# Kernel tuning notes

Hardware: AMD Instinct MI355X
Metric: run time of the kernel (lower is better)

The kernel has to match this reference:

```python
import jax, jax.numpy as jnp
import numpy as np

D = 1024      # hidden_size
FF = 4096     # ff_inner_dim = 4 * D
E = 8         # num_experts
K = 2         # moe_top_k
B, L = 4, 1024


def setup_inputs() -> dict:
    key = jax.random.key(0)
    ks = jax.random.split(key, 12)
    s = 0.02  # weight init scale
    return {
        "x": jax.random.normal(ks[0], (B, L, D), jnp.float32),
        "W_gate": jax.random.normal(ks[1], (D, E), jnp.float32) * s,
        "W1": jax.random.normal(ks[2], (E, D, FF), jnp.float32) * s,
        "b1": jnp.zeros((E, FF), jnp.float32),
        "W2": jax.random.normal(ks[3], (E, FF, D), jnp.float32) * s,
        "b2": jnp.zeros((E, D), jnp.float32),
        "Ws1": jax.random.normal(ks[4], (D, FF), jnp.float32) * s,
        "bs1": jnp.zeros((FF,), jnp.float32),
        "Ws2": jax.random.normal(ks[5], (FF, D), jnp.float32) * s,
        "bs2": jnp.zeros((D,), jnp.float32),
    }


def _gelu(h):
    # torch F.gelu default = exact (erf) gelu
    return jax.nn.gelu(h, approximate=False)


def reference(x, W_gate, W1, b1, W2, b2, Ws1, bs1, Ws2, bs2):
    Bx, Lx, Dx = x.shape
    xf = x.reshape(-1, Dx)                       # [T, D]
    logits = xf @ W_gate                         # [T, E]
    probs = jax.nn.softmax(logits, axis=-1)
    top_v, top_i = jax.lax.top_k(probs, K)       # [T, K]
    top_v = top_v / jnp.sum(top_v, axis=-1, keepdims=True)
    # dense combine weights: [T, E], zero for unselected experts
    combine = jnp.sum(jax.nn.one_hot(top_i, E, dtype=xf.dtype) * top_v[..., None], axis=1)

    out = jnp.zeros_like(xf)
    for e in range(E):  # fixed small expert loop, unrolled under jit
        h = _gelu(xf @ W1[e] + b1[e])            # [T, FF]
        out = out + combine[:, e:e + 1] * (h @ W2[e] + b2[e])

    shared = _gelu(xf @ Ws1 + bs1) @ Ws2 + bs2   # [T, D]
    return (out + shared).reshape(Bx, Lx, Dx)
```

## Files before the change

### kernel.cpp

```cpp
#include <hip/hip_runtime.h>
#include <hip/hip_bf16.h>

typedef unsigned short ushort_t;
typedef __attribute__((ext_vector_type(4))) float f32x4;
typedef __attribute__((ext_vector_type(8))) short bf16x8;
typedef __attribute__((ext_vector_type(8))) unsigned short us8;

#define T_TOK 4096
#define D_DIM 1024
#define FF_DIM 4096
#define NE 8
#define ESTRIDE 4194304L

__device__ __forceinline__ unsigned short f2bf(float f) {
  __hip_bfloat16 h = __float2bfloat16(f);
  return __builtin_bit_cast(unsigned short, h);
}
__device__ __forceinline__ float bf2f(ushort_t u) {
  unsigned int x = ((unsigned int)u) << 16;
  return __builtin_bit_cast(float, x);
}
__device__ __forceinline__ float gelu_f(float v) {
  return 0.5f * v * (1.0f + erff(v * 0.70710678118654752440f));
}

__global__ __launch_bounds__(256) void pre_kernel(
    const float* __restrict__ x, const float* __restrict__ Wg,
    const float* __restrict__ W1, const float* __restrict__ Ws1,
    int* __restrict__ cnt, int* __restrict__ tok,
    float* __restrict__ wof, int* __restrict__ rankof,
    ushort_t* __restrict__ Xbf, ushort_t* __restrict__ W1T) {
  __shared__ ushort_t tile[128][136];
  const int bid = blockIdx.x, tid = threadIdx.x;

  if (bid < 1024) {
    const int t = bid * 4 + (tid >> 6);
    const int lane = tid & 63;
    const float* xr = x + (long)t * D_DIM;
    ushort_t* xb = Xbf + (long)t * D_DIM;
    float acc[NE];
#pragma unroll
    for (int e = 0; e < NE; e++) acc[e] = 0.f;
#pragma unroll
    for (int i = 0; i < 16; i++) {
      int d = i * 64 + lane;
      float xv = xr[d];
      xb[d] = f2bf(xv);
      const float* wr = Wg + d * NE;
#pragma unroll
      for (int e = 0; e < NE; e++) acc[e] += xv * wr[e];
    }
#pragma unroll
    for (int off = 32; off > 0; off >>= 1) {
#pragma unroll
      for (int e = 0; e < NE; e++) acc[e] += __shfl_xor(acc[e], off, 64);
    }
    if (lane == 0) {
      int i0 = 0;
#pragma unroll
      for (int e = 1; e < NE; e++) if (acc[e] > acc[i0]) i0 = e;
      int i1 = -1;
#pragma unroll
      for (int e = 0; e < NE; e++) {
        if (e == i0) continue;
        if (i1 < 0 || acc[e] > acc[i1]) i1 = e;
      }
      float e1 = expf(acc[i1] - acc[i0]);
      float w0 = 1.f / (1.f + e1);
      float w1 = e1 * w0;
      int s0 = atomicAdd(&cnt[i0], 1);
      tok[i0 * T_TOK + s0] = t; wof[i0 * T_TOK + s0] = w0; rankof[i0 * T_TOK + s0] = 0;
      int s1 = atomicAdd(&cnt[i1], 1);
      tok[i1 * T_TOK + s1] = t; wof[i1 * T_TOK + s1] = w1; rankof[i1 * T_TOK + s1] = 1;
      tok[8 * T_TOK + t] = t; wof[8 * T_TOK + t] = 1.f; rankof[8 * T_TOK + t] = 0;
    }
    return;
  }

  int tix = bid - 1024;
  if (tix >= 2304) return;
  const int e = tix >> 8;
  const int rem = tix & 255;
  const int r0 = (rem >> 5) * 128, c0 = (rem & 31) * 128;
  const float* src = (e == 8) ? Ws1 : (W1 + (long)e * 4194304);
  ushort_t* d = W1T + (long)e * ESTRIDE;
#pragma unroll
  for (int i = 0; i < 16; i++) {
    int lin = tid + i * 256;
    int r = lin >> 5, c = (lin & 31) * 4;
    float4 v = *(const float4*)(src + (long)(r0 + r) * 4096 + c0 + c);
    tile[c + 0][r] = f2bf(v.x);
    tile[c + 1][r] = f2bf(v.y);
    tile[c + 2][r] = f2bf(v.z);
    tile[c + 3][r] = f2bf(v.w);
  }
  __syncthreads();
#pragma unroll
  for (int i = 0; i < 8; i++) {
    int lin = tid + i * 256;
    int cc = lin >> 4, rp = lin & 15;
    us8 v = *(const us8*)&tile[cc][rp * 8];
    *(us8*)(d + (long)(c0 + cc) * 1024 + r0 + rp * 8) = v;
  }
}

__global__ void build_queue_kernel(const int* __restrict__ cnt, int* __restrict__ base,
                                   unsigned int* __restrict__ q1,
                                   unsigned int* __restrict__ q2,
                                   int* __restrict__ nq, int* __restrict__ cnt8) {
  const int e = blockIdx.x;
  int off1 = 0, off2 = 0, tot1 = 0, tot2 = 0, M = 0;
  for (int i = 0; i < 9; i++) {
    int c = (i == 8) ? T_TOK : cnt[i];
    int m = (c + 255) >> 8;
    if (i < e) { off1 += m * 16; off2 += m * 4; }
    if (i == e) M = m;
    tot1 += m * 16; tot2 += m * 4;
  }
  for (int i = threadIdx.x; i < M * 16; i += 256) {
    int my = i >> 4, nx = i & 15;
    int ms = my >> 1, mi = my & 1, ns = nx >> 2, ni = nx & 3;
    int h = M - ms * 2; if (h > 2) h = 2;
    int pos = ms * 32 + ns * (h * 4) + mi * 4 + ni;
    q1[off1 + pos] = ((unsigned)e << 16) | ((unsigned)my << 8) | (unsigned)nx;
  }
  for (int i = threadIdx.x; i < M * 4; i += 256) {
    int my = i >> 2, nx = i & 3;
    int pos = nx * M + my;
    q2[off2 + pos] = ((unsigned)e << 16) | ((unsigned)my << 8) | (unsigned)nx;
  }
  if (e == 0 && threadIdx.x == 0) {
    nq[0] = tot1; nq[1] = tot2;
    int s = 0;
    for (int i = 0; i < NE; i++) { base[i] = s; s += cnt[i]; }
    base[8] = s;
    *cnt8 = T_TOK;
  }
}

template <int K, int N, int PHASE, bool FUSE>
__global__ __launch_bounds__(1024, 1) void gemm_kernel(
    const ushort_t* __restrict__ Abase, const ushort_t* __restrict__ WT,
    const float* __restrict__ bias_e, const float* __restrict__ bias_s,
    const int* __restrict__ cnt, const int* __restrict__ base,
    const int* __restrict__ tok, const float* __restrict__ wof,
    const int* __restrict__ rankof,
    const unsigned int* __restrict__ q, const int* __restrict__ nq_all,
    ushort_t* __restrict__ He, ushort_t* __restrict__ ybuf, float* __restrict__ out,
    const float* __restrict__ W2src, const float* __restrict__ Ws2src,
    ushort_t* __restrict__ W2Tdst) {
  __shared__ char smem[131072];
  const int tid = threadIdx.x;
  const int bid = blockIdx.x;
  const int NBLK = FUSE ? 1024 : (int)gridDim.x;

  if (FUSE && bid >= 1024) {
    int tix = bid - 1024;
    if (tix >= 2304) return;
    const int e = tix >> 8;
    const int rem = tix & 255;
    const int r0 = (rem >> 3) * 128, c0 = (rem & 7) * 128;
    const float* src = (e == 8) ? Ws2src : (W2src + (long)e * 4194304);
    ushort_t* d = W2Tdst + (long)e * ESTRIDE;
    ushort_t (*tile)[136] = (ushort_t (*)[136])smem;
#pragma unroll
    for (int i = 0; i < 4; i++) {
      int lin = tid + i * 1024;
      int r = lin >> 5, c = (lin & 31) * 4;
      float4 v = *(const float4*)(src + (long)(r0 + r) * 1024 + c0 + c);
      tile[c + 0][r] = f2bf(v.x);
      tile[c + 1][r] = f2bf(v.y);
      tile[c + 2][r] = f2bf(v.z);
      tile[c + 3][r] = f2bf(v.w);
    }
    __syncthreads();
#pragma unroll
    for (int i = 0; i < 2; i++) {
      int lin = tid + i * 1024;
      int cc = lin >> 4, rp = lin & 15;
      us8 v = *(const us8*)&tile[cc][rp * 8];
      *(us8*)(d + (long)(c0 + cc) * 4096 + r0 + rp * 8) = v;
    }
    return;
  }

  const int nq = nq_all[PHASE - 1];
  const int chunk = NBLK >> 3;
  const int vbid = (bid < (chunk << 3)) ? ((bid & 7) * chunk + (bid >> 3)) : bid;

  const int w = tid >> 6, lane = tid & 63;
  const int wm = w >> 2, wn = w & 3;
  const int lr = lane & 15, lg = lane >> 4;
  char* const lds = smem;

  const int srow = tid >> 2;
  const int cg = ((tid & 3) - (srow >> 1)) & 3;

  int offA[4], offB[4];
#pragma unroll
  for (int m = 0; m < 4; m++) {
    int r = wm * 64 + m * 16 + lr;
    offA[m] = r * 64 + (((lg + (r >> 1)) & 3) << 4);
  }
#pragma unroll
  for (int n = 0; n < 4; n++) {
    int r = wn * 64 + n * 16 + lr;
    offB[n] = r * 64 + (((lg + (r >> 1)) & 3) << 4);
  }

  constexpr int NT = K / 32;

#define STAGE(buf_, kk_)                                                        \
  do {                                                                          \
    char* dd_ = lds + (buf_) * 32768 + tid * 16;                                \
    __builtin_amdgcn_global_load_lds(                                           \
        (const __attribute__((address_space(1))) void*)(pA + (kk_)),            \
        (__attribute__((address_space(3))) void*)(dd_), 16, 0, 0);              \
    __builtin_amdgcn_global_load_lds(                                           \
        (const __attribute__((address_space(1))) void*)(pB + (kk_)),            \
        (__attribute__((address_space(3))) void*)(dd_ + 16384), 16, 0, 0);      \
  } while (0)

  for (int it = vbid; it < nq; it += NBLK) {
    const unsigned int item = q[it];
    const int e = item >> 16;
    const int m0 = ((item >> 8) & 0xff) * 256;
    const int n0 = (item & 0xff) * 256;
    const int count = cnt[e];

    int rr = m0 + srow;
    int rc = (rr < count) ? rr : 0;
    long arow;
    if (PHASE == 1) arow = tok[e * T_TOK + rc];
    else            arow = (long)base[e] + rc;
    const ushort_t* pA = Abase + arow * (long)K + cg * 8;
    const ushort_t* pB = WT + (long)e * ESTRIDE + (long)(n0 + srow) * K + cg * 8;

    f32x4 acc[4][4] = {};

    __builtin_amdgcn_s_barrier();
    asm volatile("" ::: "memory");
    STAGE(0, 0); STAGE(1, 32); STAGE(2, 64);

    for (int t = 0; t < NT; t++) {
      if (t + 3 < NT) {
        STAGE((t + 3) & 3, (t + 3) * 32);
        asm volatile("s_waitcnt vmcnt(6)" ::: "memory");
      } else if (t + 3 == NT) {
        asm volatile("s_waitcnt vmcnt(4)" ::: "memory");
      } else if (t + 2 == NT) {
        asm volatile("s_waitcnt vmcnt(2)" ::: "memory");
      } else {
        asm volatile("s_waitcnt vmcnt(0)" ::: "memory");
      }
      __builtin_amdgcn_s_barrier();
      asm volatile("" ::: "memory");

      const char* aB = lds + (t & 3) * 32768;
      const char* bB = aB + 16384;
      bf16x8 av[4], bv[4];
#pragma unroll
      for (int m = 0; m < 4; m++) av[m] = *(const bf16x8*)(aB + offA[m]);
#pragma unroll
      for (int n = 0; n < 4; n++) bv[n] = *(const bf16x8*)(bB + offB[n]);
#pragma unroll
      for (int m = 0; m < 4; m++)
#pragma unroll
        for (int n = 0; n < 4; n++)
          acc[m][n] = __builtin_amdgcn_mfma_f32_16x16x32_bf16(av[m], bv[n], acc[m][n], 0, 0, 0);

      __builtin_amdgcn_s_barrier();
      asm volatile("" ::: "memory");
    }

    const float* bias = (e == NE) ? bias_s : (bias_e + (long)e * N);
#pragma unroll
    for (int m = 0; m < 4; m++) {
#pragma unroll
      for (int j = 0; j < 4; j++) {
        int rloc = wm * 64 + m * 16 + lg * 4 + j;
        int rrr = m0 + rloc;
        if (rrr >= count) continue;
        if (PHASE == 1) {
          long orow = (long)base[e] + rrr;
#pragma unroll
          for (int n = 0; n < 4; n++) {
            int col = n0 + wn * 64 + n * 16 + lr;
            float v = acc[m][n][j] + bias[col];
            He[orow * FF_DIM + col] = f2bf(gelu_f(v));
          }
        } else {
          int tt = tok[e * T_TOK + rrr];
          if (e == NE) {
#pragma unroll
            for (int n = 0; n < 4; n++) {
              int col = n0 + wn * 64 + n * 16 + lr;
              out[(long)tt * D_DIM + col] = acc[m][n][j] + bias[col];
            }
          } else {
            float wgt = wof[e * T_TOK + rrr];
            int rk = rankof[e * T_TOK + rrr];
            ushort_t* dst = ybuf + (long)rk * ((long)T_TOK * D_DIM) + (long)tt * D_DIM;
#pragma unroll
            for (int n = 0; n < 4; n++) {
              int col = n0 + wn * 64 + n * 16 + lr;
              dst[col] = f2bf(wgt * (acc[m][n][j] + bias[col]));
            }
          }
        }
      }
    }
  }
#undef STAGE
}

__global__ void final_add_kernel(float* __restrict__ out, const ushort_t* __restrict__ ybuf) {
  long i = ((long)blockIdx.x * 256 + threadIdx.x) * 8;
  float4 a0 = *(const float4*)(out + i);
  float4 a1 = *(const float4*)(out + i + 4);
  us8 b = *(const us8*)(ybuf + i);
  us8 c = *(const us8*)(ybuf + (long)T_TOK * D_DIM + i);
  float r[8];
#pragma unroll
  for (int k = 0; k < 8; k++) r[k] = bf2f(b[k]) + bf2f(c[k]);
  a0.x += r[0]; a0.y += r[1]; a0.z += r[2]; a0.w += r[3];
  a1.x += r[4]; a1.y += r[5]; a1.z += r[6]; a1.w += r[7];
  *(float4*)(out + i) = a0;
  *(float4*)(out + i + 4) = a1;
}

extern "C" void kernel_launch(void* const* d_in, const int* in_sizes, int n_in,
                              void* d_out, int out_size, void* d_ws, size_t ws_size,
                              hipStream_t stream) {
  (void)in_sizes; (void)n_in; (void)out_size; (void)ws_size;
  const float* x   = (const float*)d_in[0];
  const float* Wg  = (const float*)d_in[1];
  const float* W1  = (const float*)d_in[2];
  const float* b1  = (const float*)d_in[3];
  const float* W2  = (const float*)d_in[4];
  const float* b2  = (const float*)d_in[5];
  const float* Ws1 = (const float*)d_in[6];
  const float* bs1 = (const float*)d_in[7];
  const float* Ws2 = (const float*)d_in[8];
  const float* bs2 = (const float*)d_in[9];
  float* out = (float*)d_out;

  char* ws = (char*)d_ws;
  int*      cnt    = (int*)(ws + 0);
  int*      base   = (int*)(ws + 64);
  int*      tok    = (int*)(ws + 256);
  float*    wof    = (float*)(ws + 256 + 147456);
  int*      rankof = (int*)(ws + 256 + 2 * 147456);
  ushort_t* Xbf    = (ushort_t*)(ws + 442624);
  ushort_t* W1T    = (ushort_t*)(ws + 8831232);
  ushort_t* W2T    = (ushort_t*)(ws + 84328704);
  ushort_t* He     = (ushort_t*)(ws + 159826176);
  int*      nq     = (int*)(ws + 260489472);
  unsigned int* q1 = (unsigned int*)(ws + 260489536);
  unsigned int* q2 = (unsigned int*)(ws + 260489536 + 32768);
  ushort_t* ybuf   = (ushort_t*)(ws + 261538048);

  hipMemsetAsync(cnt, 0, 64, stream);
  pre_kernel<<<3328, 256, 0, stream>>>(x, Wg, W1, Ws1, cnt, tok, wof, rankof, Xbf, W1T);
  build_queue_kernel<<<9, 256, 0, stream>>>(cnt, base, q1, q2, nq, &cnt[8]);
  gemm_kernel<1024, 4096, 1, true><<<3328, 1024, 0, stream>>>(
      Xbf, W1T, b1, bs1, cnt, base, tok, wof, rankof, q1, nq, He, ybuf, out,
      W2, Ws2, W2T);
  gemm_kernel<4096, 1024, 2, false><<<256, 1024, 0, stream>>>(
      He, W2T, b2, bs2, cnt, base, tok, wof, rankof, q2, nq, He, ybuf, out,
      nullptr, nullptr, nullptr);
  final_add_kernel<<<2048, 256, 0, stream>>>(out, ybuf);
}
```

Measured before the change: 507.2 us.

## Halve GEMM block size, give each wave a 128x64 tile and drop trailing barrier

The expert GEMM kernel now runs 512 threads (8 waves) per block instead of 1024. Each wave computes a 128x64 output tile with 8x4 MFMA fragments, so every B fragment read from LDS is reused across twice as many A rows. Each staging step now issues four global-to-LDS loads. The prefetch is moved after the per-step barrier, which lets the second barrier of each k-iteration be removed and cuts synchronisation. In exchange there are more accumulator VGPRs per wave and fewer waves to hide latency; the fused W2 transpose path is rescaled to the smaller block.

Measured after the change: 542.0 us. 1.07x slower.

```diff
diff --git a/kernel.cpp b/kernel.cpp
--- a/kernel.cpp
+++ b/kernel.cpp
@@ -139,7 +139,7 @@
 }
 
 template <int K, int N, int PHASE, bool FUSE>
-__global__ __launch_bounds__(1024, 1) void gemm_kernel(
+__global__ __launch_bounds__(512, 2) void gemm_kernel(
     const ushort_t* __restrict__ Abase, const ushort_t* __restrict__ WT,
     const float* __restrict__ bias_e, const float* __restrict__ bias_s,
     const int* __restrict__ cnt, const int* __restrict__ base,
@@ -164,8 +164,8 @@
     ushort_t* d = W2Tdst + (long)e * ESTRIDE;
     ushort_t (*tile)[136] = (ushort_t (*)[136])smem;
 #pragma unroll
-    for (int i = 0; i < 4; i++) {
-      int lin = tid + i * 1024;
+    for (int i = 0; i < 8; i++) {
+      int lin = tid + i * 512;
       int r = lin >> 5, c = (lin & 31) * 4;
       float4 v = *(const float4*)(src + (long)(r0 + r) * 1024 + c0 + c);
       tile[c + 0][r] = f2bf(v.x);
@@ -175,8 +175,8 @@
     }
     __syncthreads();
 #pragma unroll
-    for (int i = 0; i < 2; i++) {
-      int lin = tid + i * 1024;
+    for (int i = 0; i < 4; i++) {
+      int lin = tid + i * 512;
       int cc = lin >> 4, rp = lin & 15;
       us8 v = *(const us8*)&tile[cc][rp * 8];
       *(us8*)(d + (long)(c0 + cc) * 4096 + r0 + rp * 8) = v;
@@ -194,18 +194,18 @@
   char* const lds = smem;
 
   const int srow = tid >> 2;
-  const int cg = ((tid & 3) - (srow >> 1)) & 3;
-
-  int offA[4], offB[4];
-#pragma unroll
-  for (int m = 0; m < 4; m++) {
-    int r = wm * 64 + m * 16 + lr;
+  const int cg = ((tid & 3) - ((tid >> 3) & 3)) & 3;
+
+  int offA[8], offB[4];
+#pragma unroll
+  for (int m = 0; m < 8; m++) {
+    int r = wm * 128 + m * 16 + lr;
     offA[m] = r * 64 + (((lg + (r >> 1)) & 3) << 4);
   }
 #pragma unroll
   for (int n = 0; n < 4; n++) {
     int r = wn * 64 + n * 16 + lr;
-    offB[n] = r * 64 + (((lg + (r >> 1)) & 3) << 4);
+    offB[n] = 16384 + r * 64 + (((lg + (r >> 1)) & 3) << 4);
   }
 
   constexpr int NT = K / 32;
@@ -214,11 +214,17 @@
   do {                                                                          \
     char* dd_ = lds + (buf_) * 32768 + tid * 16;                                \
     __builtin_amdgcn_global_load_lds(                                           \
-        (const __attribute__((address_space(1))) void*)(pA + (kk_)),            \
+        (const __attribute__((address_space(1))) void*)(pA0 + (kk_)),           \
         (__attribute__((address_space(3))) void*)(dd_), 16, 0, 0);              \
     __builtin_amdgcn_global_load_lds(                                           \
-        (const __attribute__((address_space(1))) void*)(pB + (kk_)),            \
+        (const __attribute__((address_space(1))) void*)(pA1 + (kk_)),           \
+        (__attribute__((address_space(3))) void*)(dd_ + 8192), 16, 0, 0);       \
+    __builtin_amdgcn_global_load_lds(                                           \
+        (const __attribute__((address_space(1))) void*)(pB0 + (kk_)),           \
         (__attribute__((address_space(3))) void*)(dd_ + 16384), 16, 0, 0);      \
+    __builtin_amdgcn_global_load_lds(                                           \
+        (const __attribute__((address_space(1))) void*)(pB1 + (kk_)),           \
+        (__attribute__((address_space(3))) void*)(dd_ + 24576), 16, 0, 0);      \
   } while (0)
 
   for (int it = vbid; it < nq; it += NBLK) {
@@ -228,57 +234,53 @@
     const int n0 = (item & 0xff) * 256;
     const int count = cnt[e];
 
-    int rr = m0 + srow;
-    int rc = (rr < count) ? rr : 0;
-    long arow;
-    if (PHASE == 1) arow = tok[e * T_TOK + rc];
-    else            arow = (long)base[e] + rc;
-    const ushort_t* pA = Abase + arow * (long)K + cg * 8;
-    const ushort_t* pB = WT + (long)e * ESTRIDE + (long)(n0 + srow) * K + cg * 8;
-
-    f32x4 acc[4][4] = {};
+    long arow0, arow1;
+    {
+      int rr = m0 + srow;
+      int rc = (rr < count) ? rr : 0;
+      arow0 = (PHASE == 1) ? tok[e * T_TOK + rc] : ((long)base[e] + rc);
+      rr = m0 + 128 + srow;
+      rc = (rr < count) ? rr : 0;
+      arow1 = (PHASE == 1) ? tok[e * T_TOK + rc] : ((long)base[e] + rc);
+    }
+    const ushort_t* pA0 = Abase + arow0 * (long)K + cg * 8;
+    const ushort_t* pA1 = Abase + arow1 * (long)K + cg * 8;
+    const ushort_t* pB0 = WT + (long)e * ESTRIDE + (long)(n0 + srow) * K + cg * 8;
+    const ushort_t* pB1 = pB0 + 128L * K;
+
+    f32x4 acc[8][4] = {};
 
     __builtin_amdgcn_s_barrier();
     asm volatile("" ::: "memory");
     STAGE(0, 0); STAGE(1, 32); STAGE(2, 64);
 
     for (int t = 0; t < NT; t++) {
-      if (t + 3 < NT) {
-        STAGE((t + 3) & 3, (t + 3) * 32);
-        asm volatile("s_waitcnt vmcnt(6)" ::: "memory");
-      } else if (t + 3 == NT) {
-        asm volatile("s_waitcnt vmcnt(4)" ::: "memory");
-      } else if (t + 2 == NT) {
-        asm volatile("s_waitcnt vmcnt(2)" ::: "memory");
-      } else {
-        asm volatile("s_waitcnt vmcnt(0)" ::: "memory");
-      }
+      if (t + 2 < NT)      asm volatile("s_waitcnt vmcnt(8)" ::: "memory");
+      else if (t + 1 < NT) asm volatile("s_waitcnt vmcnt(4)" ::: "memory");
+      else                 asm volatile("s_waitcnt vmcnt(0)" ::: "memory");
       __builtin_amdgcn_s_barrier();
       asm volatile("" ::: "memory");
+      if (t + 3 < NT) STAGE((t + 3) & 3, (t + 3) * 32);
 
       const char* aB = lds + (t & 3) * 32768;
-      const char* bB = aB + 16384;
-      bf16x8 av[4], bv[4];
-#pragma unroll
-      for (int m = 0; m < 4; m++) av[m] = *(const bf16x8*)(aB + offA[m]);
-#pragma unroll
-      for (int n = 0; n < 4; n++) bv[n] = *(const bf16x8*)(bB + offB[n]);
-#pragma unroll
-      for (int m = 0; m < 4; m++)
+      bf16x8 av[8], bv[4];
+#pragma unroll
+      for (int m = 0; m < 8; m++) av[m] = *(const bf16x8*)(aB + offA[m]);
+#pragma unroll
+      for (int n = 0; n < 4; n++) bv[n] = *(const bf16x8*)(aB + offB[n]);
+#pragma unroll
+      for (int m = 0; m < 8; m++)
 #pragma unroll
         for (int n = 0; n < 4; n++)
           acc[m][n] = __builtin_amdgcn_mfma_f32_16x16x32_bf16(av[m], bv[n], acc[m][n], 0, 0, 0);
-
-      __builtin_amdgcn_s_barrier();
-      asm volatile("" ::: "memory");
     }
 
     const float* bias = (e == NE) ? bias_s : (bias_e + (long)e * N);
 #pragma unroll
-    for (int m = 0; m < 4; m++) {
+    for (int m = 0; m < 8; m++) {
 #pragma unroll
       for (int j = 0; j < 4; j++) {
-        int rloc = wm * 64 + m * 16 + lg * 4 + j;
+        int rloc = wm * 128 + m * 16 + lg * 4 + j;
         int rrr = m0 + rloc;
         if (rrr >= count) continue;
         if (PHASE == 1) {
@@ -363,10 +365,10 @@
   hipMemsetAsync(cnt, 0, 64, stream);
   pre_kernel<<<3328, 256, 0, stream>>>(x, Wg, W1, Ws1, cnt, tok, wof, rankof, Xbf, W1T);
   build_queue_kernel<<<9, 256, 0, stream>>>(cnt, base, q1, q2, nq, &cnt[8]);
-  gemm_kernel<1024, 4096, 1, true><<<3328, 1024, 0, stream>>>(
+  gemm_kernel<1024, 4096, 1, true><<<3328, 512, 0, stream>>>(
       Xbf, W1T, b1, bs1, cnt, base, tok, wof, rankof, q1, nq, He, ybuf, out,
       W2, Ws2, W2T);
-  gemm_kernel<4096, 1024, 2, false><<<256, 1024, 0, stream>>>(
+  gemm_kernel<4096, 1024, 2, false><<<256, 512, 0, stream>>>(
       He, W2T, b2, bs2, cnt, base, tok, wof, rankof, q2, nq, He, ybuf, out,
       nullptr, nullptr, nullptr);
   final_add_kernel<<<2048, 256, 0, stream>>>(out, ybuf);
```
